# Kernel tuning notes

Hardware: AMD Instinct MI355X
Metric: run time of the kernel (lower is better)

The kernel has to match this reference:

```python
import jax, jax.numpy as jnp
import numpy as np

BATCH, SEQ, DMODEL, DSTATE = 4, 2048, 1024, 16


def _hippo_legs(N):
    # HiPPO-LegS: A[n,k] = -sqrt(2n+1)sqrt(2k+1) for n>k, -(n+1) on diag; B[n]=sqrt(2n+1)
    n = np.arange(N)
    b = np.sqrt(2.0 * n + 1.0)
    A = -np.tril(np.outer(b, b), -1) - np.diag(n + 1.0)
    return A.astype(np.float32), b.astype(np.float32)


def setup_inputs() -> dict:
    key = jax.random.key(0)
    x = jax.random.normal(key, (BATCH, SEQ, DMODEL), dtype=jnp.float32)
    A_c, B_c = _hippo_legs(DSTATE)
    dt = 1.0 / float(SEQ)  # simple Euler discretization of the continuous HiPPO ODE
    A = jnp.eye(DSTATE, dtype=jnp.float32) + dt * jnp.asarray(A_c)
    Bvec = dt * jnp.asarray(B_c)
    return {"x": x, "A": A, "Bvec": Bvec}


def reference(x, A, Bvec):
    # x: (B, L, D); A: (N, N) discrete transition; Bvec: (N,) input map.
    # Selective-scan recurrence per channel: h_t = A h_{t-1} + Bvec * x_t, y_t = <Bvec, h_t>
    B, L, D = x.shape
    N = Bvec.shape[0]

    def step(h, xt):
        # h: (B, D, N), xt: (B, D)
        h = jnp.einsum('mn,bdn->bdm', A, h) + xt[..., None] * Bvec
        y = h @ Bvec  # (B, D)
        return h, y

    h0 = jnp.zeros((B, D, N), dtype=x.dtype)
    _, ys = jax.lax.scan(step, h0, jnp.moveaxis(x, 1, 0))  # ys: (L, B, D)
    return jnp.moveaxis(ys, 0, 1)  # (B, L, D)
```

## Files before the change

kernel.cpp:

```cpp
#include <hip/hip_runtime.h>

#define BATCH  4
#define SEQL   2048
#define DMODEL 1024
#define NST    16
#define CT     64
#define NCH    (SEQL / CT)
#define QSEG   16

#define WS_P     0
#define WS_W     1024
#define WS_KV    2048
#define WS_APOW  2176
#define WS_HIN   4096

__global__ __launch_bounds__(256) void setup_tables(const float* __restrict__ A,
                                                    const float* __restrict__ Bv,
                                                    float* __restrict__ ws) {
    __shared__ double buf0[256], buf1[256], buf2[256], buf3[256];
    __shared__ double bd[16], vtmp[16];
    double* S  = buf0;
    double* R  = buf1;
    double* Ta = buf2;
    double* Tb = buf3;
    const int t  = threadIdx.x;
    const int i  = t >> 4;
    const int kk = t & 15;
    const int delta = blockIdx.x;

    S[t] = (double)A[t];
    R[t] = (i == kk) ? 1.0 : 0.0;
    if (t < 16) bd[t] = (double)Bv[t];
    __syncthreads();

    for (int sb = 0; sb < 7; ++sb) {
        if ((delta >> sb) & 1) {
            double acc = 0.0;
            #pragma unroll
            for (int l = 0; l < 16; ++l) acc += R[i * 16 + l] * S[l * 16 + kk];
            Ta[t] = acc;
            __syncthreads();
            double* tmp = R; R = Ta; Ta = tmp;
        }
        if (sb < 6) {
            double acc = 0.0;
            #pragma unroll
            for (int l = 0; l < 16; ++l) acc += S[i * 16 + l] * S[l * 16 + kk];
            Tb[t] = acc;
            __syncthreads();
            double* tmp = S; S = Tb; Tb = tmp;
        }
    }

    if (delta < CT) {
        if (t < 16) {
            double acc = 0.0;
            #pragma unroll
            for (int k = 0; k < 16; ++k) acc += R[t * 16 + k] * bd[k];
            ws[WS_P + (CT - 1 - delta) * 16 + t] = (float)acc;
            vtmp[t] = acc;
        }
        __syncthreads();
        if (t == 0) {
            double kd = 0.0;
            for (int m = 0; m < 16; ++m) kd += bd[m] * vtmp[m];
            ws[WS_KV + 63 + delta] = (float)kd;
        }
    }
    if (delta >= 1 && t < 16) {
        double acc = 0.0;
        #pragma unroll
        for (int n = 0; n < 16; ++n) acc += bd[n] * R[n * 16 + t];
        ws[WS_W + (delta - 1) * 16 + t] = (float)acc;
    }
    if (delta == CT) ws[WS_APOW + t] = (float)R[t];
    if (delta == 0 && t < 63) ws[WS_KV + t] = 0.0f;
}

__global__ __launch_bounds__(256) void k1_chunkstate(const float* __restrict__ x,
                                                     const float* __restrict__ ws,
                                                     float* __restrict__ cbuf) {
    const int blk  = blockIdx.x;
    const int b    = blk >> 7;
    const int j    = (blk >> 2) & 31;
    const int dblk = blk & 3;
    const int d    = dblk * 256 + threadIdx.x;

    const float* P  = ws + WS_P;
    const float* xp = x + ((size_t)(b * SEQL + j * CT)) * DMODEL + d;

    float c[16];
    #pragma unroll
    for (int m = 0; m < 16; ++m) c[m] = 0.0f;

    float xa[8], xb[8];
    #pragma unroll
    for (int s = 0; s < 8; ++s) xa[s] = xp[(size_t)s * DMODEL];

    #pragma unroll
    for (int g = 0; g < 8; ++g) {
        float* cur = (g & 1) ? xb : xa;
        float* nxt = (g & 1) ? xa : xb;
        if (g < 7) {
            #pragma unroll
            for (int s = 0; s < 8; ++s)
                nxt[s] = xp[(size_t)((g + 1) * 8 + s) * DMODEL];
        }
        #pragma unroll
        for (int s = 0; s < 8; ++s) {
            const int ss = g * 8 + s;
            #pragma unroll
            for (int m = 0; m < 16; ++m)
                c[m] = fmaf(P[ss * 16 + m], cur[s], c[m]);
        }
    }

    float4* outp = (float4*)(cbuf + (((size_t)(b * NCH + j) * DMODEL) + d) * 16);
    #pragma unroll
    for (int q = 0; q < 4; ++q)
        outp[q] = make_float4(c[4 * q], c[4 * q + 1], c[4 * q + 2], c[4 * q + 3]);
}

__global__ __launch_bounds__(256) void k2_carry(const float* __restrict__ cbuf,
                                                float* __restrict__ ws) {
    const int blk = blockIdx.x;
    const int b   = blk >> 6;
    const int d0  = (blk & 63) * 16;
    const int t   = threadIdx.x;
    const int m   = t & 15;
    const int ch  = t >> 4;
    const int d   = d0 + ch;
    const int laneBase = t & 48;

    const size_t base0   = (((size_t)(b * NCH) * DMODEL) + d) * 16 + m;
    const size_t jstride = (size_t)DMODEL * 16;

    float cpre[NCH];
    #pragma unroll
    for (int j = 0; j < NCH; ++j)
        cpre[j] = cbuf[base0 + (size_t)j * jstride];

    float Arow[16];
    #pragma unroll
    for (int k = 0; k < 16; ++k) Arow[k] = ws[WS_APOW + m * 16 + k];

    float* hin = ws + WS_HIN;
    float s = 0.0f;
    #pragma unroll
    for (int j = 0; j < NCH; ++j) {
        hin[base0 + (size_t)j * jstride] = s;
        float acc = cpre[j];
        #pragma unroll
        for (int k = 0; k < 16; ++k)
            acc = fmaf(Arow[k], __shfl(s, laneBase + k, 64), acc);
        s = acc;
    }
}

template <int TT>
__device__ __forceinline__ void k3_body(const float* __restrict__ x,
                                        const float* __restrict__ ws,
                                        float* __restrict__ y,
                                        int b, int j, int d) {
    constexpr int LIM = (TT + 1) * QSEG;
    const float* W  = ws + WS_W + TT * QSEG * 16;
    const float* kv = ws + WS_KV;
    const float* hinp = ws + WS_HIN + (((size_t)(b * NCH + j) * DMODEL) + d) * 16;
    const float* xp = x + ((size_t)(b * SEQL + j * CT)) * DMODEL + d;

    float4 hv[4];
    #pragma unroll
    for (int q = 0; q < 4; ++q) hv[q] = ((const float4*)hinp)[q];
    float xa[8], xb[8];
    #pragma unroll
    for (int s = 0; s < 8; ++s) xa[s] = xp[(size_t)s * DMODEL];

    float h[16];
    #pragma unroll
    for (int q = 0; q < 4; ++q) {
        h[4 * q] = hv[q].x; h[4 * q + 1] = hv[q].y;
        h[4 * q + 2] = hv[q].z; h[4 * q + 3] = hv[q].w;
    }

    float yv[QSEG];
    #pragma unroll
    for (int i = 0; i < QSEG; ++i) {
        float acc = 0.0f;
        #pragma unroll
        for (int mm = 0; mm < 16; ++mm) acc = fmaf(W[i * 16 + mm], h[mm], acc);
        yv[i] = acc;
    }

    #pragma unroll
    for (int g = 0; g < LIM / 8; ++g) {
        float* cur = (g & 1) ? xb : xa;
        float* nxt = (g & 1) ? xa : xb;
        if (g + 1 < LIM / 8) {
            #pragma unroll
            for (int s = 0; s < 8; ++s)
                nxt[s] = xp[(size_t)((g + 1) * 8 + s) * DMODEL];
        }
        #pragma unroll
        for (int s = 0; s < 8; ++s) {
            const int ss = g * 8 + s;
            #pragma unroll
            for (int i = 0; i < QSEG; ++i)
                yv[i] = fmaf(kv[63 + TT * QSEG + i - ss], cur[s], yv[i]);
        }
    }

    float* yp = y + ((size_t)(b * SEQL + j * CT + TT * QSEG)) * DMODEL + d;
    #pragma unroll
    for (int i = 0; i < QSEG; ++i) yp[(size_t)i * DMODEL] = yv[i];
}

__global__ __launch_bounds__(256) void k3_output(const float* __restrict__ x,
                                                 const float* __restrict__ ws,
                                                 float* __restrict__ y) {
    const int blk  = blockIdx.x;
    const int b    = blk >> 9;
    const int j    = (blk >> 4) & 31;
    const int tt   = (blk >> 2) & 3;
    const int dblk = blk & 3;
    const int d    = dblk * 256 + threadIdx.x;

    switch (tt) {
        case 0: k3_body<0>(x, ws, y, b, j, d); break;
        case 1: k3_body<1>(x, ws, y, b, j, d); break;
        case 2: k3_body<2>(x, ws, y, b, j, d); break;
        default: k3_body<3>(x, ws, y, b, j, d); break;
    }
}

extern "C" void kernel_launch(void* const* d_in, const int* in_sizes, int n_in,
                              void* d_out, int out_size, void* d_ws, size_t ws_size,
                              hipStream_t stream) {
    (void)in_sizes; (void)n_in; (void)out_size; (void)ws_size;
    const float* x  = (const float*)d_in[0];
    const float* A  = (const float*)d_in[1];
    const float* Bv = (const float*)d_in[2];
    float* out = (float*)d_out;
    float* ws  = (float*)d_ws;

    setup_tables<<<65, 256, 0, stream>>>(A, Bv, ws);
    k1_chunkstate<<<512, 256, 0, stream>>>(x, ws, out);
    k2_carry<<<256, 256, 0, stream>>>(out, ws);
    k3_output<<<2048, 256, 0, stream>>>(x, ws, out);
}
```

Measured before the change: 122.2 us.

## Pair output segments per thread in k3 to share x loads; widen prefetch

k3 now has each thread compute two 16-step output segments of a chunk, a long one (3-PAIR) and a short one (PAIR), so the x loads and the carried-in state are shared between them. This balances work across blocks and halves the block count. The x prefetch groups in k1 and k3 grow from 8 to 16 rows, which raises memory-level parallelism at the cost of more registers. Fewer blocks and higher register pressure could reduce occupancy.

```diff
diff --git a/kernel.cpp b/kernel.cpp
--- a/kernel.cpp
+++ b/kernel.cpp
@@ -93,22 +93,22 @@
     #pragma unroll
     for (int m = 0; m < 16; ++m) c[m] = 0.0f;
 
-    float xa[8], xb[8];
-    #pragma unroll
-    for (int s = 0; s < 8; ++s) xa[s] = xp[(size_t)s * DMODEL];
-
-    #pragma unroll
-    for (int g = 0; g < 8; ++g) {
+    float xa[16], xb[16];
+    #pragma unroll
+    for (int s = 0; s < 16; ++s) xa[s] = xp[(size_t)s * DMODEL];
+
+    #pragma unroll
+    for (int g = 0; g < 4; ++g) {
         float* cur = (g & 1) ? xb : xa;
         float* nxt = (g & 1) ? xa : xb;
-        if (g < 7) {
-            #pragma unroll
-            for (int s = 0; s < 8; ++s)
-                nxt[s] = xp[(size_t)((g + 1) * 8 + s) * DMODEL];
-        }
-        #pragma unroll
-        for (int s = 0; s < 8; ++s) {
-            const int ss = g * 8 + s;
+        if (g < 3) {
+            #pragma unroll
+            for (int s = 0; s < 16; ++s)
+                nxt[s] = xp[(size_t)((g + 1) * 16 + s) * DMODEL];
+        }
+        #pragma unroll
+        for (int s = 0; s < 16; ++s) {
+            const int ss = g * 16 + s;
             #pragma unroll
             for (int m = 0; m < 16; ++m)
                 c[m] = fmaf(P[ss * 16 + m], cur[s], c[m]);
@@ -157,23 +157,29 @@
     }
 }
 
-template <int TT>
+template <int PAIR>
 __device__ __forceinline__ void k3_body(const float* __restrict__ x,
                                         const float* __restrict__ ws,
                                         float* __restrict__ y,
                                         int b, int j, int d) {
-    constexpr int LIM = (TT + 1) * QSEG;
-    const float* W  = ws + WS_W + TT * QSEG * 16;
-    const float* kv = ws + WS_KV;
+    constexpr int TTB  = 3 - PAIR;
+    constexpr int TTS  = PAIR;
+    constexpr int LIMB = (TTB + 1) * QSEG;
+    constexpr int LIMS = (TTS + 1) * QSEG;
+    constexpr int NB   = LIMB / 16;
+
+    const float* W    = ws + WS_W;
+    const float* kvB  = ws + WS_KV + 63 + TTB * QSEG;
+    const float* kvS  = ws + WS_KV + 63 + TTS * QSEG;
     const float* hinp = ws + WS_HIN + (((size_t)(b * NCH + j) * DMODEL) + d) * 16;
-    const float* xp = x + ((size_t)(b * SEQL + j * CT)) * DMODEL + d;
+    const float* xp   = x + ((size_t)(b * SEQL + j * CT)) * DMODEL + d;
 
     float4 hv[4];
     #pragma unroll
     for (int q = 0; q < 4; ++q) hv[q] = ((const float4*)hinp)[q];
-    float xa[8], xb[8];
-    #pragma unroll
-    for (int s = 0; s < 8; ++s) xa[s] = xp[(size_t)s * DMODEL];
+    float xa[16], xb[16];
+    #pragma unroll
+    for (int s = 0; s < 16; ++s) xa[s] = xp[(size_t)s * DMODEL];
 
     float h[16];
     #pragma unroll
@@ -182,54 +188,63 @@
         h[4 * q + 2] = hv[q].z; h[4 * q + 3] = hv[q].w;
     }
 
-    float yv[QSEG];
+    float yvB[QSEG], yvS[QSEG];
     #pragma unroll
     for (int i = 0; i < QSEG; ++i) {
-        float acc = 0.0f;
-        #pragma unroll
-        for (int mm = 0; mm < 16; ++mm) acc = fmaf(W[i * 16 + mm], h[mm], acc);
-        yv[i] = acc;
-    }
-
-    #pragma unroll
-    for (int g = 0; g < LIM / 8; ++g) {
+        float aB = 0.0f, aS = 0.0f;
+        #pragma unroll
+        for (int mm = 0; mm < 16; ++mm) {
+            aB = fmaf(W[(TTB * QSEG + i) * 16 + mm], h[mm], aB);
+            aS = fmaf(W[(TTS * QSEG + i) * 16 + mm], h[mm], aS);
+        }
+        yvB[i] = aB; yvS[i] = aS;
+    }
+
+    #pragma unroll
+    for (int g = 0; g < NB; ++g) {
         float* cur = (g & 1) ? xb : xa;
         float* nxt = (g & 1) ? xa : xb;
-        if (g + 1 < LIM / 8) {
-            #pragma unroll
-            for (int s = 0; s < 8; ++s)
-                nxt[s] = xp[(size_t)((g + 1) * 8 + s) * DMODEL];
-        }
-        #pragma unroll
-        for (int s = 0; s < 8; ++s) {
-            const int ss = g * 8 + s;
+        if (g + 1 < NB) {
+            #pragma unroll
+            for (int s = 0; s < 16; ++s)
+                nxt[s] = xp[(size_t)((g + 1) * 16 + s) * DMODEL];
+        }
+        #pragma unroll
+        for (int s = 0; s < 16; ++s) {
+            const int ss = g * 16 + s;
+            float xv = cur[s];
             #pragma unroll
             for (int i = 0; i < QSEG; ++i)
-                yv[i] = fmaf(kv[63 + TT * QSEG + i - ss], cur[s], yv[i]);
-        }
-    }
-
-    float* yp = y + ((size_t)(b * SEQL + j * CT + TT * QSEG)) * DMODEL + d;
-    #pragma unroll
-    for (int i = 0; i < QSEG; ++i) yp[(size_t)i * DMODEL] = yv[i];
+                yvB[i] = fmaf(kvB[i - ss], xv, yvB[i]);
+            if (ss < LIMS) {
+                #pragma unroll
+                for (int i = 0; i < QSEG; ++i)
+                    yvS[i] = fmaf(kvS[i - ss], xv, yvS[i]);
+            }
+        }
+    }
+
+    float* ypB = y + ((size_t)(b * SEQL + j * CT + TTB * QSEG)) * DMODEL + d;
+    float* ypS = y + ((size_t)(b * SEQL + j * CT + TTS * QSEG)) * DMODEL + d;
+    #pragma unroll
+    for (int i = 0; i < QSEG; ++i) {
+        ypB[(size_t)i * DMODEL] = yvB[i];
+        ypS[(size_t)i * DMODEL] = yvS[i];
+    }
 }
 
 __global__ __launch_bounds__(256) void k3_output(const float* __restrict__ x,
                                                  const float* __restrict__ ws,
                                                  float* __restrict__ y) {
     const int blk  = blockIdx.x;
-    const int b    = blk >> 9;
-    const int j    = (blk >> 4) & 31;
-    const int tt   = (blk >> 2) & 3;
+    const int b    = blk >> 8;
+    const int j    = (blk >> 3) & 31;
+    const int pair = (blk >> 2) & 1;
     const int dblk = blk & 3;
     const int d    = dblk * 256 + threadIdx.x;
 
-    switch (tt) {
-        case 0: k3_body<0>(x, ws, y, b, j, d); break;
-        case 1: k3_body<1>(x, ws, y, b, j, d); break;
-        case 2: k3_body<2>(x, ws, y, b, j, d); break;
-        default: k3_body<3>(x, ws, y, b, j, d); break;
-    }
+    if (pair == 0) k3_body<0>(x, ws, y, b, j, d);
+    else           k3_body<1>(x, ws, y, b, j, d);
 }
 
 extern "C" void kernel_launch(void* const* d_in, const int* in_sizes, int n_in,
@@ -245,5 +260,5 @@
     setup_tables<<<65, 256, 0, stream>>>(A, Bv, ws);
     k1_chunkstate<<<512, 256, 0, stream>>>(x, ws, out);
     k2_carry<<<256, 256, 0, stream>>>(out, ws);
-    k3_output<<<2048, 256, 0, stream>>>(x, ws, out);
-}
+    k3_output<<<1024, 256, 0, stream>>>(x, ws, out);
+}
```

Result: slower. 131.7 us (+7.8%).
